# Optimization experiments

Hardware: AMD Instinct MI355X
Metric: run time of the kernel (lower is better)

## Reference

```python
import jax, jax.numpy as jnp
import numpy as np

TEMPERATURE = 0.07
NEG_INF = -9e15
EPS = 1e-12

def setup_inputs() -> dict:
    key = jax.random.key(0)
    k1, k2 = jax.random.split(key)
    N, D = 8192, 128
    features = jax.random.normal(k1, (N, D), dtype=jnp.float32)
    labels = jax.random.randint(k2, (N,), 0, 16, dtype=jnp.int64)
    return {"features": features, "labels": labels}

def reference(features, labels):
    N = features.shape[0]
    # L2 normalize rows (torch F.normalize: x / max(||x||, eps))
    norm = jnp.linalg.norm(features, axis=1, keepdims=True)
    f = features / jnp.maximum(norm, EPS)
    # [N, N] similarity
    sim = jnp.matmul(f, f.T) / TEMPERATURE
    eye = jnp.eye(N, dtype=bool)
    sim = jnp.where(eye, NEG_INF, sim)
    # positive-pair mask: same label, excluding self
    pos_mask = ((labels[:, None] == labels[None, :]) & ~eye).astype(sim.dtype)
    denom = jnp.exp(sim).sum(axis=1, keepdims=True)  # [N, 1]
    log_prob = sim - jnp.log(denom + EPS)
    loss = -(pos_mask * log_prob).sum(axis=1) / (pos_mask.sum(axis=1) + EPS)
    return loss.mean()
```

## Files before the change

### kernel.cpp

```cpp
#include <hip/hip_runtime.h>
#include <hip/hip_bf16.h>

#define EPS 1e-12f
#define SQRT_C_EXP 4.53981597f
#define M_LN2F 0.69314718056f
#define NUM_CLASSES 16

#define BM 256
#define BN 128
#define KD 128
#define NCHUNK 8
#define PSTRIDE 32

typedef __attribute__((ext_vector_type(4))) float f32x4;
typedef __attribute__((ext_vector_type(8))) short bf16x8;

__device__ __forceinline__ float bf2f(ushort u) {
    unsigned int x = ((unsigned int)u) << 16;
    return __uint_as_float(x);
}

__device__ __forceinline__ void gload16(const void* g, void* l) {
    __builtin_amdgcn_global_load_lds(
        (const __attribute__((address_space(1))) void*)g,
        (__attribute__((address_space(3))) void*)l, 16, 0, 0);
}

__device__ __forceinline__ const bf16x8* lds_frag(const ushort* base, int r, int slot) {
    int sw = slot ^ (r & 7);
    return reinterpret_cast<const bf16x8*>(
        reinterpret_cast<const char*>(base) + r * 256 + sw * 16);
}

__global__ void normalize_kernel(const float* __restrict__ feat,
                                 const int* __restrict__ labels,
                                 ushort* __restrict__ fb,
                                 float* __restrict__ sq,
                                 float* __restrict__ cnt16,
                                 int N) {
    const int tid  = threadIdx.x;
    const int lane = tid & 63;
    const int w    = tid >> 6;
    int r = (blockIdx.x * blockDim.x + tid) >> 6;
    if (r < N) {
        const float2 v = *reinterpret_cast<const float2*>(feat + (size_t)r * KD + lane * 2);
        float s = v.x * v.x + v.y * v.y;
        #pragma unroll
        for (int off = 1; off < 64; off <<= 1) s += __shfl_xor(s, off);
        const float scale = SQRT_C_EXP / fmaxf(sqrtf(s), EPS);

        __hip_bfloat16 h0 = __float2bfloat16(v.x * scale);
        __hip_bfloat16 h1 = __float2bfloat16(v.y * scale);
        ushort u0 = *reinterpret_cast<ushort*>(&h0);
        ushort u1 = *reinterpret_cast<ushort*>(&h1);
        unsigned int pack = (unsigned int)u0 | ((unsigned int)u1 << 16);
        *reinterpret_cast<unsigned int*>(fb + (size_t)r * KD + lane * 2) = pack;

        float q0 = bf2f(u0), q1 = bf2f(u1);
        float q = q0 * q0 + q1 * q1;
        #pragma unroll
        for (int off = 1; off < 64; off <<= 1) q += __shfl_xor(q, off);
        if (lane == 0) sq[r] = q;
    }

    if (blockIdx.x == 0) {
        int cl[NUM_CLASSES];
        #pragma unroll
        for (int c = 0; c < NUM_CLASSES; c++) cl[c] = 0;
        for (int i = tid; i < N; i += 256) {
            int lb = labels[i];
            #pragma unroll
            for (int c = 0; c < NUM_CLASSES; c++) cl[c] += (lb == c) ? 1 : 0;
        }
        #pragma unroll
        for (int c = 0; c < NUM_CLASSES; c++) {
            int v = cl[c];
            #pragma unroll
            for (int off = 1; off < 64; off <<= 1) v += __shfl_xor(v, off);
            cl[c] = v;
        }
        __shared__ int hw[4][NUM_CLASSES];
        if (lane == 0) {
            #pragma unroll
            for (int c = 0; c < NUM_CLASSES; c++) hw[w][c] = cl[c];
        }
        __syncthreads();
        if (tid < NUM_CLASSES)
            cnt16[tid] = (float)(hw[0][tid] + hw[1][tid] + hw[2][tid] + hw[3][tid]);
    }
}

__global__ __launch_bounds__(512)
__attribute__((amdgpu_waves_per_eu(2, 2)))
void supcon_denom(
    const ushort* __restrict__ fb,
    const int* __restrict__ labels,
    float* __restrict__ part,
    int N) {

    __shared__ __align__(16) ushort As[BM * KD];
    __shared__ __align__(16) ushort Bs[2][BN * KD];

    const int tid  = threadIdx.x;
    const int lane = tid & 63;
    const int w    = tid >> 6;
    const int wr   = w >> 1;
    const int wc   = w & 1;
    const int r16  = lane & 15;
    const int g4   = lane >> 4;

    const int rowbase = blockIdx.y * BM;
    const int col0    = blockIdx.x * (BN * NCHUNK);

    {
        const ushort* gA = fb + (size_t)rowbase * KD;
        #pragma unroll
        for (int i = 0; i < 8; i++) {
            int d = i * 512 + tid;
            int s = d ^ ((d >> 4) & 7);
            gload16(gA + (size_t)s * 8, &As[d * 8]);
        }
        const ushort* gB = fb + (size_t)col0 * KD;
        #pragma unroll
        for (int i = 0; i < 4; i++) {
            int d = i * 512 + tid;
            int s = d ^ ((d >> 4) & 7);
            gload16(gB + (size_t)s * 8, &Bs[0][d * 8]);
        }
    }

    int rlab[4][4];
    #pragma unroll
    for (int m = 0; m < 4; m++)
        #pragma unroll
        for (int i = 0; i < 4; i++)
            rlab[m][i] = labels[rowbase + wr * 64 + m * 16 + g4 * 4 + i];

    __syncthreads();

    bf16x8 a[4][4];
    #pragma unroll
    for (int ks = 0; ks < 4; ks++) {
        const int slot = ks * 4 + g4;
        #pragma unroll
        for (int m = 0; m < 4; m++)
            a[ks][m] = *lds_frag(As, wr * 64 + m * 16 + r16, slot);
    }

    float pd[4][4], pp[4][4];
    #pragma unroll
    for (int m = 0; m < 4; m++)
        #pragma unroll
        for (int i = 0; i < 4; i++) { pd[m][i] = 0.f; pp[m][i] = 0.f; }

    int cur = 0;
    for (int c = 0; c < NCHUNK; c++) {
        if (c + 1 < NCHUNK) {
            const ushort* gB = fb + (size_t)(col0 + (c + 1) * BN) * KD;
            ushort* dstb = Bs[cur ^ 1];
            #pragma unroll
            for (int i = 0; i < 4; i++) {
                int d = i * 512 + tid;
                int s = d ^ ((d >> 4) & 7);
                gload16(gB + (size_t)s * 8, &dstb[d * 8]);
            }
        }

        const ushort* bbase = Bs[cur];
        const int colbase = col0 + c * BN + wc * 64;

        #pragma unroll 1
        for (int n2 = 0; n2 < 2; n2++) {
            int clab[2];
            #pragma unroll
            for (int j = 0; j < 2; j++)
                clab[j] = labels[colbase + (n2 * 2 + j) * 16 + r16];

            f32x4 acc[4][2];
            #pragma unroll
            for (int m = 0; m < 4; m++)
                #pragma unroll
                for (int j = 0; j < 2; j++) acc[m][j] = f32x4{0.f, 0.f, 0.f, 0.f};

            #pragma unroll
            for (int ks = 0; ks < 4; ks++) {
                const int slot = ks * 4 + g4;
                bf16x8 bv[2];
                #pragma unroll
                for (int j = 0; j < 2; j++)
                    bv[j] = *lds_frag(bbase, wc * 64 + (n2 * 2 + j) * 16 + r16, slot);
                #pragma unroll
                for (int m = 0; m < 4; m++)
                    #pragma unroll
                    for (int j = 0; j < 2; j++)
                        acc[m][j] = __builtin_amdgcn_mfma_f32_16x16x32_bf16(a[ks][m], bv[j], acc[m][j], 0, 0, 0);
            }

            #pragma unroll
            for (int m = 0; m < 4; m++)
                #pragma unroll
                for (int j = 0; j < 2; j++)
                    #pragma unroll
                    for (int i = 0; i < 4; i++) {
                        const float sim = acc[m][j][i];
                        pd[m][i] += __builtin_amdgcn_exp2f(sim);
                        pp[m][i] += (rlab[m][i] == clab[j]) ? sim : 0.f;
                    }
        }

        __syncthreads();
        cur ^= 1;
    }

    #pragma unroll
    for (int off = 1; off < 16; off <<= 1)
        #pragma unroll
        for (int m = 0; m < 4; m++)
            #pragma unroll
            for (int i = 0; i < 4; i++) {
                pd[m][i] += __shfl_xor(pd[m][i], off);
                pp[m][i] += __shfl_xor(pp[m][i], off);
            }

    if (r16 == 0) {
        const int slot = blockIdx.x * 2 + wc;
        #pragma unroll
        for (int m = 0; m < 4; m++)
            #pragma unroll
            for (int i = 0; i < 4; i++) {
                int r = rowbase + wr * 64 + m * 16 + g4 * 4 + i;
                float* p = part + (size_t)r * PSTRIDE + slot;
                p[0]  = pd[m][i];
                p[16] = pp[m][i];
            }
    }
}

__global__ void rowloss_kernel(const float* __restrict__ part,
                               const float* __restrict__ sq,
                               const int* __restrict__ labels,
                               const float* __restrict__ cnt16,
                               float* __restrict__ rowloss,
                               int N) {
    int r    = (blockIdx.x * blockDim.x + threadIdx.x) >> 6;
    int lane = threadIdx.x & 63;
    if (r >= N) return;

    float v = (lane < PSTRIDE) ? part[(size_t)r * PSTRIDE + lane] : 0.f;
    #pragma unroll
    for (int off = 1; off < 16; off <<= 1) v += __shfl_xor(v, off);
    float dsum = __shfl(v, 0);
    float psum = __shfl(v, 16);

    if (lane == 0) {
        float sqr    = sq[r];
        float possum = (psum - sqr) * M_LN2F;
        float cnt    = cnt16[labels[r]] - 1.0f;
        float dn     = dsum - __builtin_amdgcn_exp2f(sqr);
        rowloss[r]   = -(possum - cnt * logf(dn + EPS)) / (cnt + EPS);
    }
}

__global__ void reduce_kernel(const float* __restrict__ rowloss,
                              float* __restrict__ out, int N) {
    __shared__ float sdata[16];
    float s = 0.f;
    for (int r = threadIdx.x; r < N; r += blockDim.x) s += rowloss[r];
    #pragma unroll
    for (int off = 1; off < 64; off <<= 1) s += __shfl_xor(s, off);
    int wv = threadIdx.x >> 6;
    if ((threadIdx.x & 63) == 0) sdata[wv] = s;
    __syncthreads();
    if (threadIdx.x == 0) {
        float t = 0.f;
        int nw = (int)(blockDim.x >> 6);
        for (int i = 0; i < nw; i++) t += sdata[i];
        out[0] = t / (float)N;
    }
}

extern "C" void kernel_launch(void* const* d_in, const int* in_sizes, int n_in,
                              void* d_out, int out_size, void* d_ws, size_t ws_size,
                              hipStream_t stream) {
    const float* feat = (const float*)d_in[0];
    const int* labels = (const int*)d_in[1];
    const int N = in_sizes[1];

    char* ws = (char*)d_ws;
    size_t off = 0;
    ushort* fb     = (ushort*)(ws + off);  off += (size_t)N * KD * sizeof(ushort);
    float* sq      = (float*)(ws + off);   off += (size_t)N * sizeof(float);
    float* cnt16   = (float*)(ws + off);   off += (size_t)NUM_CLASSES * sizeof(float);
    float* part    = (float*)(ws + off);   off += (size_t)N * PSTRIDE * sizeof(float);
    float* rowloss = (float*)(ws + off);

    normalize_kernel<<<(N + 3) / 4, 256, 0, stream>>>(feat, labels, fb, sq, cnt16, N);

    dim3 grid(N / (BN * NCHUNK), N / BM);
    supcon_denom<<<grid, 512, 0, stream>>>(fb, labels, part, N);

    rowloss_kernel<<<(N + 3) / 4, 256, 0, stream>>>(part, sq, labels, cnt16, rowloss, N);
    reduce_kernel<<<1, 1024, 0, stream>>>(rowloss, (float*)d_out, N);
}
```

Baseline: 50.31 us.

## Shrink similarity tiles to 128x32 with 256-thread blocks and more column groups

Reshapes the fused similarity/exp-sum kernel from 512-thread blocks with 256-row by 128-column chunks into 256-thread blocks with 128-row by 32-column chunks. The grid grows to 16 column groups by 64 row groups, with three blocks allowed per CU, to raise occupancy and spread work across more CUs. The inner n2 loop is removed, so each chunk now does a single B fragment per k-step. In exchange, A tiles are reloaded more often, there is one barrier per 32 columns, and the partial buffer doubles to 64 slots per row, so the row-loss kernel reduces over 32 lanes.

```diff
diff --git a/kernel.cpp b/kernel.cpp
--- a/kernel.cpp
+++ b/kernel.cpp
@@ -6,11 +6,12 @@
 #define M_LN2F 0.69314718056f
 #define NUM_CLASSES 16
 
-#define BM 256
-#define BN 128
+#define BM 128
+#define BN 32
 #define KD 128
-#define NCHUNK 8
-#define PSTRIDE 32
+#define NCHUNK 16
+#define NCOLG 16
+#define PSTRIDE 64
 
 typedef __attribute__((ext_vector_type(4))) float f32x4;
 typedef __attribute__((ext_vector_type(8))) short bf16x8;
@@ -90,9 +91,7 @@
     }
 }
 
-__global__ __launch_bounds__(512)
-__attribute__((amdgpu_waves_per_eu(2, 2)))
-void supcon_denom(
+__global__ __launch_bounds__(256, 3) void supcon_denom(
     const ushort* __restrict__ fb,
     const int* __restrict__ labels,
     float* __restrict__ part,
@@ -116,14 +115,14 @@
         const ushort* gA = fb + (size_t)rowbase * KD;
         #pragma unroll
         for (int i = 0; i < 8; i++) {
-            int d = i * 512 + tid;
+            int d = i * 256 + tid;
             int s = d ^ ((d >> 4) & 7);
             gload16(gA + (size_t)s * 8, &As[d * 8]);
         }
         const ushort* gB = fb + (size_t)col0 * KD;
         #pragma unroll
-        for (int i = 0; i < 4; i++) {
-            int d = i * 512 + tid;
+        for (int i = 0; i < 2; i++) {
+            int d = i * 256 + tid;
             int s = d ^ ((d >> 4) & 7);
             gload16(gB + (size_t)s * 8, &Bs[0][d * 8]);
         }
@@ -159,54 +158,36 @@
             const ushort* gB = fb + (size_t)(col0 + (c + 1) * BN) * KD;
             ushort* dstb = Bs[cur ^ 1];
             #pragma unroll
-            for (int i = 0; i < 4; i++) {
-                int d = i * 512 + tid;
+            for (int i = 0; i < 2; i++) {
+                int d = i * 256 + tid;
                 int s = d ^ ((d >> 4) & 7);
                 gload16(gB + (size_t)s * 8, &dstb[d * 8]);
             }
         }
 
+        const int clab = labels[col0 + c * BN + wc * 16 + r16];
+
+        f32x4 acc[4];
+        #pragma unroll
+        for (int m = 0; m < 4; m++) acc[m] = f32x4{0.f, 0.f, 0.f, 0.f};
+
         const ushort* bbase = Bs[cur];
-        const int colbase = col0 + c * BN + wc * 64;
-
-        #pragma unroll 1
-        for (int n2 = 0; n2 < 2; n2++) {
-            int clab[2];
-            #pragma unroll
-            for (int j = 0; j < 2; j++)
-                clab[j] = labels[colbase + (n2 * 2 + j) * 16 + r16];
-
-            f32x4 acc[4][2];
+        #pragma unroll
+        for (int ks = 0; ks < 4; ks++) {
+            bf16x8 bv = *lds_frag(bbase, wc * 16 + r16, ks * 4 + g4);
             #pragma unroll
             for (int m = 0; m < 4; m++)
-                #pragma unroll
-                for (int j = 0; j < 2; j++) acc[m][j] = f32x4{0.f, 0.f, 0.f, 0.f};
-
-            #pragma unroll
-            for (int ks = 0; ks < 4; ks++) {
-                const int slot = ks * 4 + g4;
-                bf16x8 bv[2];
-                #pragma unroll
-                for (int j = 0; j < 2; j++)
-                    bv[j] = *lds_frag(bbase, wc * 64 + (n2 * 2 + j) * 16 + r16, slot);
-                #pragma unroll
-                for (int m = 0; m < 4; m++)
-                    #pragma unroll
-                    for (int j = 0; j < 2; j++)
-                        acc[m][j] = __builtin_amdgcn_mfma_f32_16x16x32_bf16(a[ks][m], bv[j], acc[m][j], 0, 0, 0);
-            }
-
-            #pragma unroll
-            for (int m = 0; m < 4; m++)
-                #pragma unroll
-                for (int j = 0; j < 2; j++)
-                    #pragma unroll
-                    for (int i = 0; i < 4; i++) {
-                        const float sim = acc[m][j][i];
-                        pd[m][i] += __builtin_amdgcn_exp2f(sim);
-                        pp[m][i] += (rlab[m][i] == clab[j]) ? sim : 0.f;
-                    }
-        }
+                acc[m] = __builtin_amdgcn_mfma_f32_16x16x32_bf16(a[ks][m], bv, acc[m], 0, 0, 0);
+        }
+
+        #pragma unroll
+        for (int m = 0; m < 4; m++)
+            #pragma unroll
+            for (int i = 0; i < 4; i++) {
+                const float sim = acc[m][i];
+                pd[m][i] += __builtin_amdgcn_exp2f(sim);
+                pp[m][i] += (rlab[m][i] == clab) ? sim : 0.f;
+            }
 
         __syncthreads();
         cur ^= 1;
@@ -231,7 +212,7 @@
                 int r = rowbase + wr * 64 + m * 16 + g4 * 4 + i;
                 float* p = part + (size_t)r * PSTRIDE + slot;
                 p[0]  = pd[m][i];
-                p[16] = pp[m][i];
+                p[32] = pp[m][i];
             }
     }
 }
@@ -246,11 +227,11 @@
     int lane = threadIdx.x & 63;
     if (r >= N) return;
 
-    float v = (lane < PSTRIDE) ? part[(size_t)r * PSTRIDE + lane] : 0.f;
-    #pragma unroll
-    for (int off = 1; off < 16; off <<= 1) v += __shfl_xor(v, off);
+    float v = part[(size_t)r * PSTRIDE + lane];
+    #pragma unroll
+    for (int off = 1; off < 32; off <<= 1) v += __shfl_xor(v, off);
     float dsum = __shfl(v, 0);
-    float psum = __shfl(v, 16);
+    float psum = __shfl(v, 32);
 
     if (lane == 0) {
         float sqr    = sq[r];
@@ -296,8 +277,8 @@
 
     normalize_kernel<<<(N + 3) / 4, 256, 0, stream>>>(feat, labels, fb, sq, cnt16, N);
 
-    dim3 grid(N / (BN * NCHUNK), N / BM);
-    supcon_denom<<<grid, 512, 0, stream>>>(fb, labels, part, N);
+    dim3 grid(NCOLG, N / BM);
+    supcon_denom<<<grid, 256, 0, stream>>>(fb, labels, part, N);
 
     rowloss_kernel<<<(N + 3) / 4, 256, 0, stream>>>(part, sq, labels, cnt16, rowloss, N);
     reduce_kernel<<<1, 1024, 0, stream>>>(rowloss, (float*)d_out, N);
```

Result: slower. 53.38 us (+6.1%).
